# Optimization experiments

Measured on AMD Instinct MI355X. Metric: run time of the kernel, lower is better.

The kernel has to match this reference:

```python
import jax, jax.numpy as jnp
import numpy as np

WS = 7          # window_size
DIM = 384
H = 12          # num_heads
N = WS * WS     # tokens per window
NW = 64         # number of windows (attn_mask.shape[0])
B_ = 4096       # window-batch; divisible by NW


def _relative_position_index(ws: int) -> np.ndarray:
    coords = np.stack(np.meshgrid(np.arange(ws), np.arange(ws), indexing='ij'))  # (2, ws, ws)
    flat = coords.reshape(2, -1)                                                 # (2, N)
    rel = flat[:, :, None] - flat[:, None, :]                                    # (2, N, N)
    rel = rel.transpose(1, 2, 0).astype(np.int64)                                # (N, N, 2)
    rel[:, :, 0] += ws - 1
    rel[:, :, 1] += ws - 1
    rel[:, :, 0] *= 2 * ws - 1
    return rel.sum(-1)                                                           # (N, N)

REL_IDX = jnp.asarray(_relative_position_index(WS))


def setup_inputs() -> dict:
    key = jax.random.key(0)
    ks = jax.random.split(key, 7)
    return {
        'x': jax.random.normal(ks[0], (B_, N, DIM), jnp.float32),
        'attn_mask': jax.random.normal(ks[1], (NW, N, N), jnp.float32),
        'qkv_w': jax.random.normal(ks[2], (3 * DIM, DIM), jnp.float32) * 0.02,
        'qkv_b': jax.random.normal(ks[3], (3 * DIM,), jnp.float32) * 0.02,
        'proj_w': jax.random.normal(ks[4], (DIM, DIM), jnp.float32) * 0.02,
        'proj_b': jax.random.normal(ks[5], (DIM,), jnp.float32) * 0.02,
        'rpb_table': jax.random.normal(ks[6], ((2 * WS - 1) ** 2, H), jnp.float32) * 0.02,
    }


def reference(x, attn_mask, qkv_w, qkv_b, proj_w, proj_b, rpb_table):
    b, n, c = x.shape
    hd = c // H
    scale = hd ** (-0.5)
    qkv = x @ qkv_w.T + qkv_b                                  # (B_, N, 3C)
    qkv = qkv.reshape(b, n, 3, H, hd).transpose(2, 0, 3, 1, 4)  # (3, B_, H, N, hd)
    q, k, v = qkv[0] * scale, qkv[1], qkv[2]
    attn = jnp.einsum('bhnd,bhmd->bhnm', q, k)                 # (B_, H, N, N)
    bias = rpb_table[REL_IDX]                                  # (N, N, H)
    attn = attn + bias.transpose(2, 0, 1)[None]
    nw = attn_mask.shape[0]
    attn = attn.reshape(b // nw, nw, H, n, n) + attn_mask[None, :, None]
    attn = jax.nn.softmax(attn.reshape(b, H, n, n), axis=-1)
    out = jnp.einsum('bhnm,bhmd->bhnd', attn, v)               # (B_, H, N, hd)
    out = out.transpose(0, 2, 1, 3).reshape(b, n, c)
    return out @ proj_w.T + proj_b
```

## Files before the change

### kernel.cpp

```cpp
#include <hip/hip_runtime.h>

#define TOKS 49
#define DIM_ 384
#define NHEAD 12
#define HDIM 32

typedef short bf16x8 __attribute__((ext_vector_type(8)));
typedef float f32x4 __attribute__((ext_vector_type(4)));

#define SXA 392
#define SQK 136
#define SV   72

#define LDS_ELEMS (64*SXA + 64*SQK + 64*SQK + 128*SV + 64*SXA)
#define LDS_BYTES (LDS_ELEMS*2)

#define W1E (3*DIM_*DIM_)
#define W2E (DIM_*DIM_)
#define CMBE (64*NHEAD*64*64)
#define WS_NEEDED ((size_t)(W1E+W2E)*2 + (size_t)CMBE*4)

__device__ __forceinline__ unsigned short f2b(float f) {
  union { float f; unsigned u; } x; x.f = f;
  return (unsigned short)((x.u + 0x7FFFu + ((x.u >> 16) & 1u)) >> 16);
}

__global__ void prep_kernel(const float* __restrict__ qkv_w,
                            const float* __restrict__ proj_w,
                            const float* __restrict__ rpb,
                            const float* __restrict__ mask,
                            unsigned short* __restrict__ w1p,
                            unsigned short* __restrict__ w2p,
                            float* __restrict__ cmb) {
  int i = blockIdx.x * 256 + threadIdx.x;
  if (i < W1E) {
    int j = i & 7, l = (i >> 3) & 63, rest = i >> 9;
    int kk = rest % 12, ct = rest / 12;
    w1p[i] = f2b(qkv_w[(ct*16 + (l & 15))*DIM_ + kk*32 + ((l >> 4) << 3) + j]);
  }
  if (i < W2E) {
    int j = i & 7, l = (i >> 3) & 63, rest = i >> 9;
    int kk = rest % 12, ct = rest / 12;
    w2p[i] = f2b(proj_w[(ct*16 + (l & 15))*DIM_ + kk*32 + ((l >> 4) << 3) + j]);
  }
  if (i < CMBE) {
    int q = i & 63, k = (i >> 6) & 63, hw = i >> 12;
    int h = hw % 12, wi = hw / 12;
    float v = -1e30f;
    if (q < TOKS && k < TOKS) {
      int idx = (q/7 - k/7 + 6)*13 + (q%7 - k%7 + 6);
      v = rpb[idx*NHEAD + h] + mask[((size_t)wi*TOKS + q)*TOKS + k];
    }
    cmb[i] = v;
  }
}

__global__ __launch_bounds__(1024, 1)
void wattn_kernel(const float* __restrict__ x,
                  const unsigned short* __restrict__ w1p,
                  const float* __restrict__ b1,
                  const unsigned short* __restrict__ w2p,
                  const float* __restrict__ b2,
                  const float* __restrict__ cmb,
                  float* __restrict__ out) {
  extern __shared__ unsigned short lds[];
  unsigned short* xA  = lds;
  unsigned short* Q4  = xA + 64*SXA;
  unsigned short* K4  = Q4 + 64*SQK;
  unsigned short* Vt4 = K4 + 64*SQK;
  unsigned short* Ob  = Vt4 + 128*SV;

  const int tid  = threadIdx.x;
  const int lane = tid & 63;
  const int wv   = tid >> 6;
  const int lr   = lane & 15;
  const int lg   = lane >> 4;
  const int b    = blockIdx.x;
  const int wi   = b & 63;

  const int mh    = wv & 1;
  const int ctile = wv >> 1;

  {
    const float* xg = x + (size_t)b * TOKS * DIM_;
    for (int idx = tid; idx < TOKS*48; idx += 1024) {
      int r = idx / 48, c8 = (idx % 48) << 3;
      const float4* p = (const float4*)(xg + r*DIM_ + c8);
      float4 a0 = p[0], a1 = p[1];
      bf16x8 v;
      v[0]=(short)f2b(a0.x); v[1]=(short)f2b(a0.y); v[2]=(short)f2b(a0.z); v[3]=(short)f2b(a0.w);
      v[4]=(short)f2b(a1.x); v[5]=(short)f2b(a1.y); v[6]=(short)f2b(a1.z); v[7]=(short)f2b(a1.w);
      *(bf16x8*)&xA[r*SXA + c8] = v;
    }
    bf16x8 z = {0,0,0,0,0,0,0,0};
    for (int idx = tid; idx < 15*48; idx += 1024) {
      int r = 49 + idx / 48, c8 = (idx % 48) << 3;
      *(bf16x8*)&xA[r*SXA + c8] = z;
    }
  }
  __syncthreads();

  const f32x4 fz = {0.f, 0.f, 0.f, 0.f};

  for (int g = 0; g < 3; ++g) {
    const int hbase = g * 4;

    {
      const int cb = hbase*2 + ctile;
      const unsigned short* bq = w1p + (size_t)(cb*12)*512 + lane*8;
      const unsigned short* bk = bq + (size_t)(24*12)*512;
      const unsigned short* bv = bq + (size_t)(48*12)*512;
      f32x4 aq[2], ak[2], av[2];
      #pragma unroll
      for (int m = 0; m < 2; ++m) { aq[m]=fz; ak[m]=fz; av[m]=fz; }
      #pragma unroll
      for (int kk = 0; kk < 12; ++kk) {
        bf16x8 fq = *(const bf16x8*)(bq + kk*512);
        bf16x8 fk = *(const bf16x8*)(bk + kk*512);
        bf16x8 fv = *(const bf16x8*)(bv + kk*512);
        #pragma unroll
        for (int m = 0; m < 2; ++m) {
          bf16x8 a = *(const bf16x8*)&xA[((mh*2 + m)*16 + lr)*SXA + kk*32 + lg*8];
          aq[m] = __builtin_amdgcn_mfma_f32_16x16x32_bf16(a, fq, aq[m], 0, 0, 0);
          ak[m] = __builtin_amdgcn_mfma_f32_16x16x32_bf16(a, fk, ak[m], 0, 0, 0);
          av[m] = __builtin_amdgcn_mfma_f32_16x16x32_bf16(a, fv, av[m], 0, 0, 0);
        }
      }
      const float bsq = b1[cb*16 + lr];
      const float bsk = b1[(24 + cb)*16 + lr];
      const float bsv = b1[(48 + cb)*16 + lr];
      const int d128 = (ctile << 4) + lr;
      #pragma unroll
      for (int m = 0; m < 2; ++m) {
        #pragma unroll
        for (int j = 0; j < 4; ++j) {
          const int tok = (mh*2 + m)*16 + lg*4 + j;
          Q4[tok*SQK + d128]  = f2b((aq[m][j] + bsq) * 0.17677669529663687f);
          K4[tok*SQK + d128]  = f2b(ak[m][j] + bsk);
          Vt4[d128*SV + tok]  = f2b(av[m][j] + bsv);
        }
      }
    }
    __syncthreads();

    {
      const int hl = wv >> 2;
      const int h  = hbase + hl;
      const int qoff = hl * HDIM;
      const int m0 = (wv & 3) << 4;

      float c[4][4];
      const float* cp = cmb + ((size_t)(wi*NHEAD + h) << 12) + m0 + lr;
      #pragma unroll
      for (int nt = 0; nt < 4; ++nt)
        #pragma unroll
        for (int jj = 0; jj < 4; ++jj)
          c[nt][jj] = cp[(nt*16 + lg*4 + jj) << 6];

      bf16x8 qa = *(const bf16x8*)&Q4[(m0 + lr)*SQK + qoff + lg*8];
      f32x4 S[4];
      #pragma unroll
      for (int nt = 0; nt < 4; ++nt) {
        bf16x8 kb = *(const bf16x8*)&K4[((nt<<4) + lr)*SQK + qoff + lg*8];
        S[nt] = __builtin_amdgcn_mfma_f32_16x16x32_bf16(kb, qa, fz, 0, 0, 0);
      }

      float p[4][4];
      float mx = -1e30f;
      #pragma unroll
      for (int nt = 0; nt < 4; ++nt)
        #pragma unroll
        for (int jj = 0; jj < 4; ++jj) {
          p[nt][jj] = S[nt][jj] + c[nt][jj];
          mx = fmaxf(mx, p[nt][jj]);
        }
      mx = fmaxf(mx, __shfl_xor(mx, 16));
      mx = fmaxf(mx, __shfl_xor(mx, 32));
      float sum = 0.f;
      #pragma unroll
      for (int nt = 0; nt < 4; ++nt)
        #pragma unroll
        for (int jj = 0; jj < 4; ++jj) {
          float e = __expf(p[nt][jj] - mx);
          p[nt][jj] = e; sum += e;
        }
      sum += __shfl_xor(sum, 16);
      sum += __shfl_xor(sum, 32);
      const float inv = 1.0f / sum;

      unsigned pk[4][2];
      #pragma unroll
      for (int nt = 0; nt < 4; ++nt) {
        pk[nt][0] = (unsigned)f2b(p[nt][0]*inv) | ((unsigned)f2b(p[nt][1]*inv) << 16);
        pk[nt][1] = (unsigned)f2b(p[nt][2]*inv) | ((unsigned)f2b(p[nt][3]*inv) << 16);
      }

      const int src0 = (lane & 15) + ((lane & 16) << 1);
      const int src1 = src0 + 16;
      const bool loH = lane < 32;
      f32x4 o0 = fz, o1 = fz;
      #pragma unroll
      for (int kk = 0; kk < 2; ++kk) {
        unsigned wA0 = __shfl(pk[2*kk][0], src0), wB0 = __shfl(pk[2*kk+1][0], src0);
        unsigned wA1 = __shfl(pk[2*kk][1], src0), wB1 = __shfl(pk[2*kk+1][1], src0);
        unsigned wA2 = __shfl(pk[2*kk][0], src1), wB2 = __shfl(pk[2*kk+1][0], src1);
        unsigned wA3 = __shfl(pk[2*kk][1], src1), wB3 = __shfl(pk[2*kk+1][1], src1);
        union { unsigned u[4]; bf16x8 v; } af;
        af.u[0] = loH ? wA0 : wB0;
        af.u[1] = loH ? wA1 : wB1;
        af.u[2] = loH ? wA2 : wB2;
        af.u[3] = loH ? wA3 : wB3;
        bf16x8 vb0 = *(const bf16x8*)&Vt4[(qoff + lr)*SV + kk*32 + lg*8];
        bf16x8 vb1 = *(const bf16x8*)&Vt4[(qoff + 16 + lr)*SV + kk*32 + lg*8];
        o0 = __builtin_amdgcn_mfma_f32_16x16x32_bf16(af.v, vb0, o0, 0, 0, 0);
        o1 = __builtin_amdgcn_mfma_f32_16x16x32_bf16(af.v, vb1, o1, 0, 0, 0);
      }
      const int ocol = h*HDIM + lr;
      #pragma unroll
      for (int j = 0; j < 4; ++j) {
        const int tok = m0 + lg*4 + j;
        Ob[tok*SXA + ocol]      = f2b(o0[j]);
        Ob[tok*SXA + ocol + 16] = f2b(o1[j]);
      }
    }
    __syncthreads();
  }

  {
    const unsigned short* bp0 = w2p + (size_t)(ctile*12)*512 + lane*8;
    const unsigned short* bp1 = bp0 + (size_t)(8*12)*512;
    const unsigned short* bp2 = bp0 + (size_t)(16*12)*512;
    f32x4 ac0[2], ac1[2], ac2[2];
    #pragma unroll
    for (int m = 0; m < 2; ++m) { ac0[m]=fz; ac1[m]=fz; ac2[m]=fz; }
    #pragma unroll
    for (int kk = 0; kk < 12; ++kk) {
      bf16x8 f0 = *(const bf16x8*)(bp0 + kk*512);
      bf16x8 f1 = *(const bf16x8*)(bp1 + kk*512);
      bf16x8 f2 = *(const bf16x8*)(bp2 + kk*512);
      #pragma unroll
      for (int m = 0; m < 2; ++m) {
        bf16x8 a = *(const bf16x8*)&Ob[((mh*2 + m)*16 + lr)*SXA + kk*32 + lg*8];
        ac0[m] = __builtin_amdgcn_mfma_f32_16x16x32_bf16(a, f0, ac0[m], 0, 0, 0);
        ac1[m] = __builtin_amdgcn_mfma_f32_16x16x32_bf16(a, f1, ac1[m], 0, 0, 0);
        ac2[m] = __builtin_amdgcn_mfma_f32_16x16x32_bf16(a, f2, ac2[m], 0, 0, 0);
      }
    }
    float* og = out + (size_t)b * TOKS * DIM_;
    #pragma unroll
    for (int ni = 0; ni < 3; ++ni) {
      const int col = ((ctile + ni*8) << 4) + lr;
      const float pb = b2[col];
      const f32x4* ac = ni == 0 ? ac0 : (ni == 1 ? ac1 : ac2);
      #pragma unroll
      for (int m = 0; m < 2; ++m)
        #pragma unroll
        for (int j = 0; j < 4; ++j) {
          const int tok = (mh*2 + m)*16 + lg*4 + j;
          if (tok < TOKS) og[tok*DIM_ + col] = ac[m][j] + pb;
        }
    }
  }
}

extern "C" void kernel_launch(void* const* d_in, const int* in_sizes, int n_in,
                              void* d_out, int out_size, void* d_ws, size_t ws_size,
                              hipStream_t stream) {
  const float* x      = (const float*)d_in[0];
  const float* mask   = (const float*)d_in[1];
  const float* qkv_w  = (const float*)d_in[2];
  const float* qkv_b  = (const float*)d_in[3];
  const float* proj_w = (const float*)d_in[4];
  const float* proj_b = (const float*)d_in[5];
  const float* rpb    = (const float*)d_in[6];
  float* out = (float*)d_out;

  if (ws_size < WS_NEEDED) return;

  unsigned short* w1p = (unsigned short*)d_ws;
  unsigned short* w2p = w1p + W1E;
  float* cmb = (float*)(w2p + W2E);

  prep_kernel<<<(CMBE + 255)/256, 256, 0, stream>>>(qkv_w, proj_w, rpb, mask,
                                                    w1p, w2p, cmb);

  hipFuncSetAttribute((const void*)wattn_kernel,
                      hipFuncAttributeMaxDynamicSharedMemorySize, LDS_BYTES);
  wattn_kernel<<<4096, 1024, LDS_BYTES, stream>>>(x, w1p, qkv_b, w2p,
                                                  proj_b, cmb, out);
}
```

Baseline: 597.8 us.

## Swap MFMA operand order to vectorize LDS and global stores

Swaps the A/B operands of several MFMAs so each lane's accumulator holds four consecutive columns rather than four consecutive rows. Q/K/V, attention-output and final-output writes become packed uint2 or float4 stores instead of scalar ones. The combined bias/mask table is transposed so each lane loads its bias with float4 loads, and the bias vectors are read as f32x4. The aim is fewer LDS and global store and load instructions, with better coalescing of the output write. It keeps the same tiling and synchronization.

New measurement: 606.0 us. About the same (+1.4%).

```diff
diff --git a/kernel.cpp b/kernel.cpp
--- a/kernel.cpp
+++ b/kernel.cpp
@@ -3,7 +3,6 @@
 #define TOKS 49
 #define DIM_ 384
 #define NHEAD 12
-#define HDIM 32
 
 typedef short bf16x8 __attribute__((ext_vector_type(8)));
 typedef float f32x4 __attribute__((ext_vector_type(4)));
@@ -23,6 +22,10 @@
 __device__ __forceinline__ unsigned short f2b(float f) {
   union { float f; unsigned u; } x; x.f = f;
   return (unsigned short)((x.u + 0x7FFFu + ((x.u >> 16) & 1u)) >> 16);
+}
+
+__device__ __forceinline__ unsigned pack2(float lo, float hi) {
+  return (unsigned)f2b(lo) | ((unsigned)f2b(hi) << 16);
 }
 
 __global__ void prep_kernel(const float* __restrict__ qkv_w,
@@ -44,7 +47,7 @@
     w2p[i] = f2b(proj_w[(ct*16 + (l & 15))*DIM_ + kk*32 + ((l >> 4) << 3) + j]);
   }
   if (i < CMBE) {
-    int q = i & 63, k = (i >> 6) & 63, hw = i >> 12;
+    int k = i & 63, q = (i >> 6) & 63, hw = i >> 12;
     int h = hw % 12, wi = hw / 12;
     float v = -1e30f;
     if (q < TOKS && k < TOKS) {
@@ -87,178 +90,186 @@
       int r = idx / 48, c8 = (idx % 48) << 3;
       const float4* p = (const float4*)(xg + r*DIM_ + c8);
       float4 a0 = p[0], a1 = p[1];
-      bf16x8 v;
-      v[0]=(short)f2b(a0.x); v[1]=(short)f2b(a0.y); v[2]=(short)f2b(a0.z); v[3]=(short)f2b(a0.w);
-      v[4]=(short)f2b(a1.x); v[5]=(short)f2b(a1.y); v[6]=(short)f2b(a1.z); v[7]=(short)f2b(a1.w);
-      *(bf16x8*)&xA[r*SXA + c8] = v;
-    }
-    bf16x8 z = {0,0,0,0,0,0,0,0};
+      uint4 w;
+      w.x = pack2(a0.x, a0.y); w.y = pack2(a0.z, a0.w);
+      w.z = pack2(a1.x, a1.y); w.w = pack2(a1.z, a1.w);
+      *(uint4*)&xA[r*SXA + c8] = w;
+    }
+    uint4 z = {0,0,0,0};
     for (int idx = tid; idx < 15*48; idx += 1024) {
       int r = 49 + idx / 48, c8 = (idx % 48) << 3;
-      *(bf16x8*)&xA[r*SXA + c8] = z;
+      *(uint4*)&xA[r*SXA + c8] = z;
     }
   }
   __syncthreads();
 
   const f32x4 fz = {0.f, 0.f, 0.f, 0.f};
+  f32x4 aq[2], ak[2], av[2];
+
+  auto g1c = [&](int gg) {
+    const int cb = gg*8 + ctile;
+    const unsigned short* bq = w1p + (size_t)(cb*12)*512 + (lane << 3);
+    const unsigned short* bk = bq + (size_t)(24*12)*512;
+    const unsigned short* bv = bq + (size_t)(48*12)*512;
+    #pragma unroll
+    for (int t = 0; t < 2; ++t) { aq[t] = fz; ak[t] = fz; av[t] = fz; }
+    #pragma unroll
+    for (int kk = 0; kk < 12; ++kk) {
+      bf16x8 fq = *(const bf16x8*)(bq + kk*512);
+      bf16x8 fk = *(const bf16x8*)(bk + kk*512);
+      bf16x8 fv = *(const bf16x8*)(bv + kk*512);
+      #pragma unroll
+      for (int t = 0; t < 2; ++t) {
+        bf16x8 a = *(const bf16x8*)&xA[((mh*2 + t)*16 + lr)*SXA + kk*32 + lg*8];
+        aq[t] = __builtin_amdgcn_mfma_f32_16x16x32_bf16(fq, a, aq[t], 0, 0, 0);
+        ak[t] = __builtin_amdgcn_mfma_f32_16x16x32_bf16(fk, a, ak[t], 0, 0, 0);
+        av[t] = __builtin_amdgcn_mfma_f32_16x16x32_bf16(a, fv, av[t], 0, 0, 0);
+      }
+    }
+  };
+
+  auto g1w = [&](int gg) {
+    const int cb = gg*8 + ctile;
+    const f32x4 qb4 = *(const f32x4*)(b1 + cb*16 + (lg << 2));
+    const f32x4 kb4 = *(const f32x4*)(b1 + (24 + cb)*16 + (lg << 2));
+    const float bsv = b1[(48 + cb)*16 + lr];
+    const int d128 = (ctile << 4) + lr;
+    #pragma unroll
+    for (int t = 0; t < 2; ++t) {
+      const int tokr = mh*32 + t*16 + lr;
+      uint2 qw, kw, vw;
+      qw.x = pack2((aq[t][0] + qb4[0]) * 0.17677669529663687f,
+                   (aq[t][1] + qb4[1]) * 0.17677669529663687f);
+      qw.y = pack2((aq[t][2] + qb4[2]) * 0.17677669529663687f,
+                   (aq[t][3] + qb4[3]) * 0.17677669529663687f);
+      kw.x = pack2(ak[t][0] + kb4[0], ak[t][1] + kb4[1]);
+      kw.y = pack2(ak[t][2] + kb4[2], ak[t][3] + kb4[3]);
+      vw.x = pack2(av[t][0] + bsv, av[t][1] + bsv);
+      vw.y = pack2(av[t][2] + bsv, av[t][3] + bsv);
+      *(uint2*)&Q4[tokr*SQK + (ctile << 4) + (lg << 2)] = qw;
+      *(uint2*)&K4[tokr*SQK + (ctile << 4) + (lg << 2)] = kw;
+      *(uint2*)&Vt4[d128*SV + mh*32 + t*16 + (lg << 2)] = vw;
+    }
+  };
 
   for (int g = 0; g < 3; ++g) {
-    const int hbase = g * 4;
-
-    {
-      const int cb = hbase*2 + ctile;
-      const unsigned short* bq = w1p + (size_t)(cb*12)*512 + lane*8;
-      const unsigned short* bk = bq + (size_t)(24*12)*512;
-      const unsigned short* bv = bq + (size_t)(48*12)*512;
-      f32x4 aq[2], ak[2], av[2];
-      #pragma unroll
-      for (int m = 0; m < 2; ++m) { aq[m]=fz; ak[m]=fz; av[m]=fz; }
-      #pragma unroll
-      for (int kk = 0; kk < 12; ++kk) {
-        bf16x8 fq = *(const bf16x8*)(bq + kk*512);
-        bf16x8 fk = *(const bf16x8*)(bk + kk*512);
-        bf16x8 fv = *(const bf16x8*)(bv + kk*512);
-        #pragma unroll
-        for (int m = 0; m < 2; ++m) {
-          bf16x8 a = *(const bf16x8*)&xA[((mh*2 + m)*16 + lr)*SXA + kk*32 + lg*8];
-          aq[m] = __builtin_amdgcn_mfma_f32_16x16x32_bf16(a, fq, aq[m], 0, 0, 0);
-          ak[m] = __builtin_amdgcn_mfma_f32_16x16x32_bf16(a, fk, ak[m], 0, 0, 0);
-          av[m] = __builtin_amdgcn_mfma_f32_16x16x32_bf16(a, fv, av[m], 0, 0, 0);
-        }
-      }
-      const float bsq = b1[cb*16 + lr];
-      const float bsk = b1[(24 + cb)*16 + lr];
-      const float bsv = b1[(48 + cb)*16 + lr];
-      const int d128 = (ctile << 4) + lr;
-      #pragma unroll
-      for (int m = 0; m < 2; ++m) {
-        #pragma unroll
-        for (int j = 0; j < 4; ++j) {
-          const int tok = (mh*2 + m)*16 + lg*4 + j;
-          Q4[tok*SQK + d128]  = f2b((aq[m][j] + bsq) * 0.17677669529663687f);
-          K4[tok*SQK + d128]  = f2b(ak[m][j] + bsk);
-          Vt4[d128*SV + tok]  = f2b(av[m][j] + bsv);
-        }
-      }
-    }
+    g1c(g);
+    g1w(g);
     __syncthreads();
 
-    {
-      const int hl = wv >> 2;
-      const int h  = hbase + hl;
-      const int qoff = hl * HDIM;
-      const int m0 = (wv & 3) << 4;
-
-      float c[4][4];
-      const float* cp = cmb + ((size_t)(wi*NHEAD + h) << 12) + m0 + lr;
-      #pragma unroll
-      for (int nt = 0; nt < 4; ++nt)
-        #pragma unroll
-        for (int jj = 0; jj < 4; ++jj)
-          c[nt][jj] = cp[(nt*16 + lg*4 + jj) << 6];
-
-      bf16x8 qa = *(const bf16x8*)&Q4[(m0 + lr)*SQK + qoff + lg*8];
-      f32x4 S[4];
-      #pragma unroll
-      for (int nt = 0; nt < 4; ++nt) {
-        bf16x8 kb = *(const bf16x8*)&K4[((nt<<4) + lr)*SQK + qoff + lg*8];
-        S[nt] = __builtin_amdgcn_mfma_f32_16x16x32_bf16(kb, qa, fz, 0, 0, 0);
-      }
-
-      float p[4][4];
-      float mx = -1e30f;
-      #pragma unroll
-      for (int nt = 0; nt < 4; ++nt)
-        #pragma unroll
-        for (int jj = 0; jj < 4; ++jj) {
-          p[nt][jj] = S[nt][jj] + c[nt][jj];
-          mx = fmaxf(mx, p[nt][jj]);
-        }
-      mx = fmaxf(mx, __shfl_xor(mx, 16));
-      mx = fmaxf(mx, __shfl_xor(mx, 32));
-      float sum = 0.f;
-      #pragma unroll
-      for (int nt = 0; nt < 4; ++nt)
-        #pragma unroll
-        for (int jj = 0; jj < 4; ++jj) {
-          float e = __expf(p[nt][jj] - mx);
-          p[nt][jj] = e; sum += e;
-        }
-      sum += __shfl_xor(sum, 16);
-      sum += __shfl_xor(sum, 32);
-      const float inv = 1.0f / sum;
-
-      unsigned pk[4][2];
-      #pragma unroll
-      for (int nt = 0; nt < 4; ++nt) {
-        pk[nt][0] = (unsigned)f2b(p[nt][0]*inv) | ((unsigned)f2b(p[nt][1]*inv) << 16);
-        pk[nt][1] = (unsigned)f2b(p[nt][2]*inv) | ((unsigned)f2b(p[nt][3]*inv) << 16);
-      }
-
-      const int src0 = (lane & 15) + ((lane & 16) << 1);
-      const int src1 = src0 + 16;
-      const bool loH = lane < 32;
-      f32x4 o0 = fz, o1 = fz;
-      #pragma unroll
-      for (int kk = 0; kk < 2; ++kk) {
-        unsigned wA0 = __shfl(pk[2*kk][0], src0), wB0 = __shfl(pk[2*kk+1][0], src0);
-        unsigned wA1 = __shfl(pk[2*kk][1], src0), wB1 = __shfl(pk[2*kk+1][1], src0);
-        unsigned wA2 = __shfl(pk[2*kk][0], src1), wB2 = __shfl(pk[2*kk+1][0], src1);
-        unsigned wA3 = __shfl(pk[2*kk][1], src1), wB3 = __shfl(pk[2*kk+1][1], src1);
-        union { unsigned u[4]; bf16x8 v; } af;
-        af.u[0] = loH ? wA0 : wB0;
-        af.u[1] = loH ? wA1 : wB1;
-        af.u[2] = loH ? wA2 : wB2;
-        af.u[3] = loH ? wA3 : wB3;
-        bf16x8 vb0 = *(const bf16x8*)&Vt4[(qoff + lr)*SV + kk*32 + lg*8];
-        bf16x8 vb1 = *(const bf16x8*)&Vt4[(qoff + 16 + lr)*SV + kk*32 + lg*8];
-        o0 = __builtin_amdgcn_mfma_f32_16x16x32_bf16(af.v, vb0, o0, 0, 0, 0);
-        o1 = __builtin_amdgcn_mfma_f32_16x16x32_bf16(af.v, vb1, o1, 0, 0, 0);
-      }
-      const int ocol = h*HDIM + lr;
-      #pragma unroll
-      for (int j = 0; j < 4; ++j) {
-        const int tok = m0 + lg*4 + j;
-        Ob[tok*SXA + ocol]      = f2b(o0[j]);
-        Ob[tok*SXA + ocol + 16] = f2b(o1[j]);
-      }
-    }
+    const int hl = wv >> 2;
+    const int h  = g*4 + hl;
+    const int qoff = hl * 32;
+    const int m0 = (wv & 3) << 4;
+
+    f32x4 c4[4];
+    const float* cp = cmb + (((size_t)(wi*NHEAD + h)) << 12) + ((m0 + lr) << 6);
+    #pragma unroll
+    for (int nt = 0; nt < 4; ++nt)
+      c4[nt] = *(const f32x4*)(cp + nt*16 + (lg << 2));
+
+    bf16x8 qa = *(const bf16x8*)&Q4[(m0 + lr)*SQK + qoff + lg*8];
+    f32x4 S[4];
+    #pragma unroll
+    for (int nt = 0; nt < 4; ++nt) {
+      bf16x8 kb = *(const bf16x8*)&K4[((nt << 4) + lr)*SQK + qoff + lg*8];
+      S[nt] = __builtin_amdgcn_mfma_f32_16x16x32_bf16(kb, qa, fz, 0, 0, 0);
+    }
+
+    float p[4][4];
+    float mx = -1e30f;
+    #pragma unroll
+    for (int nt = 0; nt < 4; ++nt)
+      #pragma unroll
+      for (int jj = 0; jj < 4; ++jj) {
+        p[nt][jj] = S[nt][jj] + c4[nt][jj];
+        mx = fmaxf(mx, p[nt][jj]);
+      }
+    mx = fmaxf(mx, __shfl_xor(mx, 16));
+    mx = fmaxf(mx, __shfl_xor(mx, 32));
+    float sum = 0.f;
+    #pragma unroll
+    for (int nt = 0; nt < 4; ++nt)
+      #pragma unroll
+      for (int jj = 0; jj < 4; ++jj) {
+        float e = __expf(p[nt][jj] - mx);
+        p[nt][jj] = e; sum += e;
+      }
+    sum += __shfl_xor(sum, 16);
+    sum += __shfl_xor(sum, 32);
+    const float inv = 1.0f / sum;
+
+    unsigned pk0[4], pk1[4];
+    #pragma unroll
+    for (int nt = 0; nt < 4; ++nt) {
+      pk0[nt] = pack2(p[nt][0]*inv, p[nt][1]*inv);
+      pk1[nt] = pack2(p[nt][2]*inv, p[nt][3]*inv);
+    }
+
+    const int src0 = lr + ((lane & 16) << 1);
+    const int src1 = src0 + 16;
+    const bool loH = lane < 32;
+    f32x4 o0 = fz, o1 = fz;
+    #pragma unroll
+    for (int kk = 0; kk < 2; ++kk) {
+      unsigned wA0 = __shfl(pk0[2*kk], src0), wB0 = __shfl(pk0[2*kk+1], src0);
+      unsigned wA1 = __shfl(pk1[2*kk], src0), wB1 = __shfl(pk1[2*kk+1], src0);
+      unsigned wA2 = __shfl(pk0[2*kk], src1), wB2 = __shfl(pk0[2*kk+1], src1);
+      unsigned wA3 = __shfl(pk1[2*kk], src1), wB3 = __shfl(pk1[2*kk+1], src1);
+      union { unsigned u[4]; bf16x8 v; } af;
+      af.u[0] = loH ? wA0 : wB0;
+      af.u[1] = loH ? wA1 : wB1;
+      af.u[2] = loH ? wA2 : wB2;
+      af.u[3] = loH ? wA3 : wB3;
+      bf16x8 vb0 = *(const bf16x8*)&Vt4[(qoff + lr)*SV + kk*32 + lg*8];
+      bf16x8 vb1 = *(const bf16x8*)&Vt4[(qoff + 16 + lr)*SV + kk*32 + lg*8];
+      o0 = __builtin_amdgcn_mfma_f32_16x16x32_bf16(vb0, af.v, o0, 0, 0, 0);
+      o1 = __builtin_amdgcn_mfma_f32_16x16x32_bf16(vb1, af.v, o1, 0, 0, 0);
+    }
+    const int orow = m0 + lr;
+    uint2 w0, w1;
+    w0.x = pack2(o0[0], o0[1]); w0.y = pack2(o0[2], o0[3]);
+    w1.x = pack2(o1[0], o1[1]); w1.y = pack2(o1[2], o1[3]);
+    *(uint2*)&Ob[orow*SXA + h*32 + (lg << 2)]      = w0;
+    *(uint2*)&Ob[orow*SXA + h*32 + 16 + (lg << 2)] = w1;
+
     __syncthreads();
   }
 
   {
-    const unsigned short* bp0 = w2p + (size_t)(ctile*12)*512 + lane*8;
+    const unsigned short* bp0 = w2p + (size_t)(ctile*12)*512 + (lane << 3);
     const unsigned short* bp1 = bp0 + (size_t)(8*12)*512;
     const unsigned short* bp2 = bp0 + (size_t)(16*12)*512;
     f32x4 ac0[2], ac1[2], ac2[2];
     #pragma unroll
-    for (int m = 0; m < 2; ++m) { ac0[m]=fz; ac1[m]=fz; ac2[m]=fz; }
+    for (int t = 0; t < 2; ++t) { ac0[t] = fz; ac1[t] = fz; ac2[t] = fz; }
     #pragma unroll
     for (int kk = 0; kk < 12; ++kk) {
       bf16x8 f0 = *(const bf16x8*)(bp0 + kk*512);
       bf16x8 f1 = *(const bf16x8*)(bp1 + kk*512);
       bf16x8 f2 = *(const bf16x8*)(bp2 + kk*512);
       #pragma unroll
-      for (int m = 0; m < 2; ++m) {
-        bf16x8 a = *(const bf16x8*)&Ob[((mh*2 + m)*16 + lr)*SXA + kk*32 + lg*8];
-        ac0[m] = __builtin_amdgcn_mfma_f32_16x16x32_bf16(a, f0, ac0[m], 0, 0, 0);
-        ac1[m] = __builtin_amdgcn_mfma_f32_16x16x32_bf16(a, f1, ac1[m], 0, 0, 0);
-        ac2[m] = __builtin_amdgcn_mfma_f32_16x16x32_bf16(a, f2, ac2[m], 0, 0, 0);
+      for (int t = 0; t < 2; ++t) {
+        bf16x8 ob = *(const bf16x8*)&Ob[((mh*2 + t)*16 + lr)*SXA + kk*32 + lg*8];
+        ac0[t] = __builtin_amdgcn_mfma_f32_16x16x32_bf16(f0, ob, ac0[t], 0, 0, 0);
+        ac1[t] = __builtin_amdgcn_mfma_f32_16x16x32_bf16(f1, ob, ac1[t], 0, 0, 0);
+        ac2[t] = __builtin_amdgcn_mfma_f32_16x16x32_bf16(f2, ob, ac2[t], 0, 0, 0);
       }
     }
     float* og = out + (size_t)b * TOKS * DIM_;
     #pragma unroll
     for (int ni = 0; ni < 3; ++ni) {
-      const int col = ((ctile + ni*8) << 4) + lr;
-      const float pb = b2[col];
+      const int col0 = ((ctile + ni*8) << 4) + (lg << 2);
+      const f32x4 pb = *(const f32x4*)(b2 + col0);
       const f32x4* ac = ni == 0 ? ac0 : (ni == 1 ? ac1 : ac2);
       #pragma unroll
-      for (int m = 0; m < 2; ++m)
-        #pragma unroll
-        for (int j = 0; j < 4; ++j) {
-          const int tok = (mh*2 + m)*16 + lg*4 + j;
-          if (tok < TOKS) og[tok*DIM_ + col] = ac[m][j] + pb;
+      for (int t = 0; t < 2; ++t) {
+        const int tok = (mh*2 + t)*16 + lr;
+        if (tok < TOKS) {
+          f32x4 v = ac[t] + pb;
+          *(f32x4*)(og + tok*DIM_ + col0) = v;
         }
+      }
     }
   }
 }
```
